# Performance work log

Measured on AMD Instinct MI355X. Metric: run time of the kernel, lower is better.

The kernel has to match this reference:

```python
import jax, jax.numpy as jnp
import numpy as np

EPS = 1e-5

def _conv3x3(x, w):
    # x: [n,c,h,w], w: [o,c,3,3], stride 1, padding 1 (SAME)
    return jax.lax.conv_general_dilated(x, w, (1, 1), 'SAME',
                                        dimension_numbers=('NCHW', 'OIHW', 'NCHW'))

def _bn(x, g, b, m, v):
    # inference-mode BatchNorm2d with running stats
    s = g / jnp.sqrt(v + EPS)
    return x * s[:, None, None] + (b - m * s)[:, None, None]

def _lrelu(x):
    return jnp.where(x > 0, x, 0.2 * x)

def _conv1x1(x, w, b):
    # w: [o,c] (1x1 conv kernel collapsed)
    return jnp.einsum('nchw,oc->nohw', x, w) + b[:, None, None]

def _conv_relu(x, w, g, b, m, v):
    return _lrelu(_bn(_conv3x3(x, w), g, b, m, v))

def _pam(f, Wq, bq, Wk, bk, Wv, bv, alpha):
    n, c, h, w = f.shape
    hw = h * w
    q = _conv1x1(f, Wq, bq).reshape(n, -1, hw)   # [n,cr,hw]
    k = _conv1x1(f, Wk, bk).reshape(n, -1, hw)   # [n,cr,hw]
    # attention[i,j] over spatial tokens, softmax along j
    attn = jax.nn.softmax(jnp.einsum('nci,ncj->nij', q, k), axis=-1)  # [n,hw,hw]
    v = _conv1x1(f, Wv, bv).reshape(n, c, hw)    # [n,c,hw]
    # torch: bmm(v, attn^T) -> out[:, :, i] = sum_j v[:, :, j] * attn[i, j]
    out = jnp.einsum('ncj,nij->nci', v, attn).reshape(n, c, h, w)
    return alpha * out + f

def _cam(f, W1, b1, W2, b2):
    s = jnp.mean(f, axis=(2, 3), keepdims=True)  # AdaptiveAvgPool2d(1)
    s = _lrelu(_conv1x1(s, W1, b1))
    s = jax.nn.sigmoid(_conv1x1(s, W2, b2))
    return f * s

def _upx2(x):
    n, c, h, w = x.shape
    return jax.image.resize(x, (n, c, 2 * h, 2 * w), 'bilinear')

def setup_inputs() -> dict:
    key = jax.random.key(0)
    ks = jax.random.split(key, 16)
    N, C, H, W_ = 4, 512, 64, 64
    CR, NC = C // 8, 64
    f32 = jnp.float32
    def nrm(k, shape, s=0.05):
        return jax.random.normal(k, shape, f32) * s
    return {
        'x': jax.random.normal(ks[0], (N, C, H, W_), f32),
        'W_pam_in': nrm(ks[1], (C, C, 3, 3)),
        'pam_gamma': jnp.ones((C,), f32), 'pam_beta': jnp.zeros((C,), f32),
        'pam_mean': nrm(ks[2], (C,)), 'pam_var': jax.random.uniform(ks[3], (C,), f32) + 0.5,
        'Wq': nrm(ks[4], (CR, C)), 'bq': jnp.zeros((CR,), f32),
        'Wk': nrm(ks[5], (CR, C)), 'bk': jnp.zeros((CR,), f32),
        'Wv': nrm(ks[6], (C, C)), 'bv': jnp.zeros((C,), f32),
        'alpha': nrm(ks[7], (1,), 1.0),
        'W_pam_out': nrm(ks[8], (NC, C)), 'b_pam_out': jnp.zeros((NC,), f32),
        'W_cam_in': nrm(ks[9], (C, C, 3, 3)),
        'cam_gamma': jnp.ones((C,), f32), 'cam_beta': jnp.zeros((C,), f32),
        'cam_mean': nrm(ks[10], (C,)), 'cam_var': jax.random.uniform(ks[11], (C,), f32) + 0.5,
        'Wc1': nrm(ks[12], (CR, C)), 'bc1': jnp.zeros((CR,), f32),
        'Wc2': nrm(ks[13], (C, CR)), 'bc2': jnp.zeros((C,), f32),
        'W_cam_out': nrm(ks[14], (NC, C)), 'b_cam_out': jnp.zeros((NC,), f32),
    }

def reference(x, W_pam_in, pam_gamma, pam_beta, pam_mean, pam_var,
              Wq, bq, Wk, bk, Wv, bv, alpha, W_pam_out, b_pam_out,
              W_cam_in, cam_gamma, cam_beta, cam_mean, cam_var,
              Wc1, bc1, Wc2, bc2, W_cam_out, b_cam_out):
    pam_feat = _conv_relu(x, W_pam_in, pam_gamma, pam_beta, pam_mean, pam_var)
    pam_feat = _pam(pam_feat, Wq, bq, Wk, bk, Wv, bv, alpha)
    pam_feat = _upx2(_conv1x1(pam_feat, W_pam_out, b_pam_out))
    cam_feat = _conv_relu(x, W_cam_in, cam_gamma, cam_beta, cam_mean, cam_var)
    cam_feat = _cam(cam_feat, Wc1, bc1, Wc2, bc2)
    cam_feat = _upx2(_conv1x1(cam_feat, W_cam_out, b_cam_out))
    return pam_feat + cam_feat
```

## Files before the change

### kernel.cpp

```cpp
#include <hip/hip_runtime.h>
#include <hip/hip_bf16.h>
#include <math.h>

#define N_  4
#define C_  512
#define H_  64
#define W_  64
#define HW_ 4096
#define CR_ 64
#define NC_ 64
#define EPSV 1e-5f

typedef __attribute__((ext_vector_type(8))) __bf16 bf16x8;
typedef __attribute__((ext_vector_type(4))) float f32x4;
typedef __hip_bfloat16 bf16s;

__device__ __forceinline__ unsigned short bfb(float f) {
    union { bf16s h; unsigned short u; } cv;
    cv.h = __float2bfloat16(f);
    return cv.u;
}

__device__ __forceinline__ int swz8(int row, int ch) {
    return row * 64 + ((ch ^ (row & 7)) << 3);
}

__global__ __launch_bounds__(256) void k_xpose(
    const float* __restrict__ x, bf16s* __restrict__ xbT)
{
    __shared__ float xs[64][65];
    const int tid = threadIdx.x;
    const int n = blockIdx.z, c0 = blockIdx.y * 64, p0 = blockIdx.x * 64;
    for (int e = tid; e < 4096; e += 256) {
        int ci = e >> 6, pi = e & 63;
        xs[ci][pi] = x[((size_t)(n*C_ + c0 + ci))*HW_ + p0 + pi];
    }
    __syncthreads();
    for (int e = tid; e < 4096; e += 256) {
        int pi = e >> 6, ci = e & 63;
        xbT[((size_t)n*HW_ + p0 + pi)*C_ + c0 + ci] = __float2bfloat16(xs[ci][pi]);
    }
}

__global__ __launch_bounds__(256) void k_wprep(
    const float* __restrict__ w, bf16s* __restrict__ wb)
{
    int e = blockIdx.x * 256 + threadIdx.x;
    int c = e & 511; int r = e >> 9;
    int tap = r % 9; int o = r / 9;
    wb[e] = __float2bfloat16(w[((size_t)o*C_ + c)*9 + tap]);
}

__global__ __launch_bounds__(256) void k_wcast(
    const float* __restrict__ in, bf16s* __restrict__ out, int nElem)
{
    int e = blockIdx.x * 256 + threadIdx.x;
    if (e < nElem) out[e] = __float2bfloat16(in[e]);
}

__global__ __launch_bounds__(256, 2) void k_conv3x3_mfma(
    const bf16s* __restrict__ xbT, const bf16s* __restrict__ wb,
    const float* __restrict__ gamma, const float* __restrict__ beta,
    const float* __restrict__ mean, const float* __restrict__ var,
    float* __restrict__ out, bf16s* __restrict__ featT,
    float* __restrict__ csum, int mode)
{
    __shared__ bf16s aL[3][128][40];
    __shared__ bf16s bL[132][40];
    const int tid = threadIdx.x;
    const int n  = blockIdx.z;
    const int o0 = blockIdx.y * 128;
    const int pt = blockIdx.x;
    const int y0 = pt * 2;
    const int lane = tid & 63;
    const int wid  = tid >> 6;
    const int wr = wid >> 1, wc = wid & 1;
    const int lr = lane & 15, cb = lane >> 4;

    const int ao  = tid >> 2;
    const int ac  = (tid & 3) * 8;
    const int t0  = tid >> 2;
    const int t1  = t0 + 64;
    const int t2  = t0 + 128;
    const int ry1 = t1 >= 66 ? 1 : 0;
    const int xi1 = t1 - (ry1 ? 66 : 0);

    f32x4 acc[4][4];
#pragma unroll
    for (int i = 0; i < 4; ++i)
#pragma unroll
        for (int j = 0; j < 4; ++j) acc[i][j] = (f32x4){0.f,0.f,0.f,0.f};

    int4 pA0, pA1, pA2, pA3, pA4, pA5, pB0, pB1, pB2;

#define CONV_AADDR(DXI, OHALF, C0, DYI) \
    (const int4*)(wb + ((size_t)(o0 + (OHALF) + ao)*9 + (DYI)*3 + (DXI))*C_ + (C0) + ac)

#define CONV_BLOAD(DST, RY, XI, C0, DYI, VALID)                               \
    {                                                                         \
        int row_ = y0 + (DYI) - 1 + (RY);                                     \
        int xc_  = (XI) - 1;                                                  \
        int4 v_ = {0,0,0,0};                                                  \
        if ((VALID) && row_ >= 0 && row_ < H_ && xc_ >= 0 && xc_ < W_)        \
            v_ = *(const int4*)(xbT +                                         \
                ((size_t)n*HW_ + row_*W_ + xc_)*C_ + (C0) + ac);              \
        DST = v_;                                                             \
    }

#define CONV_ISSUE(C0, DYI)                                                   \
    {                                                                         \
        pA0 = *CONV_AADDR(0,  0, C0, DYI);                                    \
        pA1 = *CONV_AADDR(0, 64, C0, DYI);                                    \
        pA2 = *CONV_AADDR(1,  0, C0, DYI);                                    \
        pA3 = *CONV_AADDR(1, 64, C0, DYI);                                    \
        pA4 = *CONV_AADDR(2,  0, C0, DYI);                                    \
        pA5 = *CONV_AADDR(2, 64, C0, DYI);                                    \
        CONV_BLOAD(pB0, 0, t0, C0, DYI, 1)                                    \
        CONV_BLOAD(pB1, ry1, xi1, C0, DYI, 1)                                 \
        CONV_BLOAD(pB2, 1, t2 - 66, C0, DYI, tid < 16)                        \
    }

    CONV_ISSUE(0, 0)
    int c0 = 0, dyi = 0;
    for (int it = 0; it < 48; ++it) {
        *(int4*)&aL[0][ao][ac]      = pA0;
        *(int4*)&aL[0][64 + ao][ac] = pA1;
        *(int4*)&aL[1][ao][ac]      = pA2;
        *(int4*)&aL[1][64 + ao][ac] = pA3;
        *(int4*)&aL[2][ao][ac]      = pA4;
        *(int4*)&aL[2][64 + ao][ac] = pA5;
        *(int4*)&bL[t0][ac] = pB0;
        *(int4*)&bL[t1][ac] = pB1;
        if (tid < 16) *(int4*)&bL[t2][ac] = pB2;
        __syncthreads();
        int nd = dyi + 1, nc = c0;
        if (nd == 3) { nd = 0; nc += 32; }
        if (it < 47) CONV_ISSUE(nc, nd)
#pragma unroll
        for (int dxi = 0; dxi < 3; ++dxi) {
            bf16x8 af[4], bfv[4];
#pragma unroll
            for (int fm = 0; fm < 4; ++fm)
                af[fm] = *(const bf16x8*)&aL[dxi][wr*64 + fm*16 + lr][cb*8];
#pragma unroll
            for (int fn = 0; fn < 4; ++fn) {
                int pg = wc*64 + fn*16 + lr;
                int ry = pg >> 6, xc = pg & 63;
                bfv[fn] = *(const bf16x8*)&bL[ry*66 + xc + dxi][cb*8];
            }
#pragma unroll
            for (int fm = 0; fm < 4; ++fm)
#pragma unroll
                for (int fn = 0; fn < 4; ++fn)
                    acc[fm][fn] = __builtin_amdgcn_mfma_f32_16x16x32_bf16(
                        af[fm], bfv[fn], acc[fm][fn], 0, 0, 0);
        }
        __syncthreads();
        c0 = nc; dyi = nd;
    }
#undef CONV_ISSUE
#undef CONV_BLOAD
#undef CONV_AADDR
#pragma unroll
    for (int fm = 0; fm < 4; ++fm) {
        float sc[4], sh[4];
        const int obase = o0 + wr*64 + fm*16 + cb*4;
#pragma unroll
        for (int r = 0; r < 4; ++r) {
            int o = obase + r;
            sc[r] = gamma[o] * rsqrtf(var[o] + EPSV);
            sh[r] = beta[o] - mean[o]*sc[r];
        }
        float ps[4] = {0.f, 0.f, 0.f, 0.f};
#pragma unroll
        for (int fn = 0; fn < 4; ++fn) {
            int pg = wc*64 + fn*16 + lr;
            int p  = pt*128 + pg;
            float vv[4];
#pragma unroll
            for (int r = 0; r < 4; ++r) {
                float t = fmaf(acc[fm][fn][r], sc[r], sh[r]);
                vv[r] = t > 0.f ? t : 0.2f*t;
                if (mode == 0)
                    out[((size_t)(n*C_ + obase + r))*HW_ + p] = vv[r];
                else
                    ps[r] += vv[r];
            }
            uint2 u;
            u.x = (unsigned)bfb(vv[0]) | ((unsigned)bfb(vv[1]) << 16);
            u.y = (unsigned)bfb(vv[2]) | ((unsigned)bfb(vv[3]) << 16);
            *(uint2*)&featT[((size_t)n*HW_ + p)*C_ + obase] = u;
        }
        if (mode != 0) {
#pragma unroll
            for (int r = 0; r < 4; ++r) {
                float s = ps[r];
                s += __shfl_xor(s, 1);
                s += __shfl_xor(s, 2);
                s += __shfl_xor(s, 4);
                s += __shfl_xor(s, 8);
                if (lr == 0) atomicAdd(&csum[n*C_ + obase + r], s);
            }
        }
    }
}

__global__ __launch_bounds__(256, 2) void k_gemm(
    const bf16s* __restrict__ A, const bf16s* __restrict__ Bt,
    const float* __restrict__ bias, const float* __restrict__ scale,
    void* __restrict__ outp, int O, int mode)
{
    __shared__ bf16s aL[64][40];
    __shared__ bf16s bL[256][40];
    const int tid = threadIdx.x;
    const int n  = blockIdx.z;
    const int p0 = blockIdx.x * 256;
    const int o0 = blockIdx.y * 64;
    const int lane = tid & 63;
    const int wid  = tid >> 6;
    const int lr = lane & 15, cb = lane >> 4;
    const int arow = tid >> 2, ach = (tid & 3) * 8;

    f32x4 acc[4][4];
#pragma unroll
    for (int i = 0; i < 4; ++i)
#pragma unroll
        for (int j = 0; j < 4; ++j) acc[i][j] = (f32x4){0.f,0.f,0.f,0.f};

    int4 pA, pB0, pB1, pB2, pB3;
    float4 pS0, pS1;

#define GEMM_ISSUE(C0)                                                        \
    {                                                                         \
        pA = *(const int4*)&A[(size_t)(o0 + arow)*C_ + (C0) + ach];           \
        if (scale) {                                                          \
            pS0 = *(const float4*)&scale[(size_t)n*C_ + (C0) + ach];          \
            pS1 = *(const float4*)&scale[(size_t)n*C_ + (C0) + ach + 4];      \
        }                                                                     \
        pB0 = *(const int4*)&Bt[((size_t)n*HW_ + p0 + arow      )*C_ + (C0) + ach]; \
        pB1 = *(const int4*)&Bt[((size_t)n*HW_ + p0 + arow +  64)*C_ + (C0) + ach]; \
        pB2 = *(const int4*)&Bt[((size_t)n*HW_ + p0 + arow + 128)*C_ + (C0) + ach]; \
        pB3 = *(const int4*)&Bt[((size_t)n*HW_ + p0 + arow + 192)*C_ + (C0) + ach]; \
    }

    GEMM_ISSUE(0)
    for (int c0 = 0; c0 < C_; c0 += 32) {
        if (scale) {
            const bf16s* sp = (const bf16s*)&pA;
            bf16s tmp[8];
            tmp[0] = __float2bfloat16(__bfloat162float(sp[0]) * pS0.x);
            tmp[1] = __float2bfloat16(__bfloat162float(sp[1]) * pS0.y);
            tmp[2] = __float2bfloat16(__bfloat162float(sp[2]) * pS0.z);
            tmp[3] = __float2bfloat16(__bfloat162float(sp[3]) * pS0.w);
            tmp[4] = __float2bfloat16(__bfloat162float(sp[4]) * pS1.x);
            tmp[5] = __float2bfloat16(__bfloat162float(sp[5]) * pS1.y);
            tmp[6] = __float2bfloat16(__bfloat162float(sp[6]) * pS1.z);
            tmp[7] = __float2bfloat16(__bfloat162float(sp[7]) * pS1.w);
            *(int4*)&aL[arow][ach] = *(int4*)tmp;
        } else {
            *(int4*)&aL[arow][ach] = pA;
        }
        *(int4*)&bL[arow      ][ach] = pB0;
        *(int4*)&bL[arow +  64][ach] = pB1;
        *(int4*)&bL[arow + 128][ach] = pB2;
        *(int4*)&bL[arow + 192][ach] = pB3;
        __syncthreads();
        if (c0 + 32 < C_) GEMM_ISSUE(c0 + 32)
        bf16x8 af[4], bfv[4];
#pragma unroll
        for (int fo = 0; fo < 4; ++fo)
            af[fo] = *(const bf16x8*)&aL[fo*16 + lr][cb*8];
#pragma unroll
        for (int fp = 0; fp < 4; ++fp)
            bfv[fp] = *(const bf16x8*)&bL[wid*64 + fp*16 + lr][cb*8];
#pragma unroll
        for (int fo = 0; fo < 4; ++fo)
#pragma unroll
            for (int fp = 0; fp < 4; ++fp)
                acc[fo][fp] = __builtin_amdgcn_mfma_f32_16x16x32_bf16(
                    af[fo], bfv[fp], acc[fo][fp], 0, 0, 0);
        __syncthreads();
    }
#undef GEMM_ISSUE
#pragma unroll
    for (int fo = 0; fo < 4; ++fo) {
        const int obase = o0 + fo*16 + cb*4;
        float bv[4];
#pragma unroll
        for (int r = 0; r < 4; ++r) bv[r] = bias[obase + r];
#pragma unroll
        for (int fp = 0; fp < 4; ++fp) {
            int p = p0 + wid*64 + fp*16 + lr;
            float v[4];
#pragma unroll
            for (int r = 0; r < 4; ++r) v[r] = acc[fo][fp][r] + bv[r];
            if (mode == 1) {
                uint2 u;
                u.x = (unsigned)bfb(v[0]) | ((unsigned)bfb(v[1]) << 16);
                u.y = (unsigned)bfb(v[2]) | ((unsigned)bfb(v[3]) << 16);
                *(uint2*)&((bf16s*)outp)[((size_t)n*HW_ + p)*O + (obase - o0)] = u;
            } else if (mode == 2) {
#pragma unroll
                for (int r = 0; r < 4; ++r)
                    ((bf16s*)outp)[((size_t)(n*O + obase + r))*HW_ + p] =
                        __float2bfloat16(v[r]);
            } else {
#pragma unroll
                for (int r = 0; r < 4; ++r)
                    ((float*)outp)[((size_t)(n*O + obase + r))*HW_ + p] = v[r];
            }
        }
    }
}

__global__ __launch_bounds__(256) void k_rowstats_mfma(
    const bf16s* __restrict__ qb, const bf16s* __restrict__ kb,
    float* __restrict__ rowm, float* __restrict__ rowl)
{
    __shared__ bf16s qs[4096];
    __shared__ bf16s ks[4096];
    const int tid = threadIdx.x;
    const int lid = blockIdx.x + (blockIdx.y << 6) + (blockIdx.z << 8);
    const int n  = lid & 3;
    const int jz = (lid >> 2) & 1;
    const int i0 = (lid >> 3) << 6;
    const int lane = tid & 63;
    const int wid  = tid >> 6;
    const int lr = lane & 15, cb = lane >> 4;

    for (int e = tid; e < 512; e += 256) {
        int row = e >> 3, ch = e & 7;
        *(int4*)&qs[swz8(row, ch)] =
            *(const int4*)&qb[((size_t)n*HW_ + i0 + row)*CR_ + ch*8];
    }
    const int krow = tid >> 3, kch = tid & 7;
    const bf16s* kbase = kb + (size_t)n*HW_*CR_ + (size_t)jz*2048*CR_ + kch*8;
    int4 kreg0 = *(const int4*)(kbase + (size_t)krow*CR_);
    int4 kreg1 = *(const int4*)(kbase + (size_t)(krow + 32)*CR_);
    __syncthreads();
    bf16x8 bq[2];
#pragma unroll
    for (int kk = 0; kk < 2; ++kk)
        bq[kk] = *(const bf16x8*)&qs[swz8(wid*16 + lr, kk*4 + cb)];

    float m_t = -INFINITY, l_t = 0.f;
    for (int t = 0; t < 32; ++t) {
        __syncthreads();
        *(int4*)&ks[swz8(krow, kch)] = kreg0;
        *(int4*)&ks[swz8(krow + 32, kch)] = kreg1;
        if (t < 31) {
            kreg0 = *(const int4*)(kbase + (size_t)((t+1)*64 + krow)*CR_);
            kreg1 = *(const int4*)(kbase + (size_t)((t+1)*64 + krow + 32)*CR_);
        }
        __syncthreads();
        f32x4 sv[4];
#pragma unroll
        for (int fj = 0; fj < 4; ++fj) {
            f32x4 s = (f32x4){0.f,0.f,0.f,0.f};
#pragma unroll
            for (int kk = 0; kk < 2; ++kk) {
                bf16x8 ak = *(const bf16x8*)&ks[swz8(fj*16 + lr, kk*4 + cb)];
                s = __builtin_amdgcn_mfma_f32_16x16x32_bf16(ak, bq[kk], s, 0, 0, 0);
            }
            sv[fj] = s;
        }
        float mx = m_t;
#pragma unroll
        for (int fj = 0; fj < 4; ++fj)
#pragma unroll
            for (int r = 0; r < 4; ++r) mx = fmaxf(mx, sv[fj][r]);
        float sum = 0.f;
#pragma unroll
        for (int fj = 0; fj < 4; ++fj)
#pragma unroll
            for (int r = 0; r < 4; ++r) sum += __expf(sv[fj][r] - mx);
        l_t = l_t * __expf(m_t - mx) + sum;
        m_t = mx;
    }
#pragma unroll
    for (int mask = 16; mask <= 32; mask <<= 1) {
        float mo = __shfl_xor(m_t, mask);
        float lo = __shfl_xor(l_t, mask);
        float m2 = fmaxf(m_t, mo);
        l_t = l_t * __expf(m_t - m2) + lo * __expf(mo - m2);
        m_t = m2;
    }
    if (cb == 0) {
        rowm[((size_t)jz*N_ + n)*HW_ + i0 + wid*16 + lr] = m_t;
        rowl[((size_t)jz*N_ + n)*HW_ + i0 + wid*16 + lr] = l_t;
    }
}

__global__ __launch_bounds__(256, 4) void k_pv_mfma(
    const bf16s* __restrict__ qb, const bf16s* __restrict__ kb,
    const bf16s* __restrict__ vb, const float* __restrict__ rowm,
    const float* __restrict__ rowl, const float* __restrict__ alpha,
    const float* __restrict__ feat, bf16s* __restrict__ featT)
{
    __shared__ bf16s ks[4096];
    __shared__ bf16s qps[4096];
    const int tid = threadIdx.x;
    const int lid = blockIdx.x + (blockIdx.y << 6) + (blockIdx.z << 8);
    const int k8  = lid & 7;
    const int n   = k8 >> 1;
    const int cc0 = (((lid >> 3) & 1) * 2 + (k8 & 1)) << 7;
    const int i0  = (lid >> 4) << 6;
    const int lane = tid & 63;
    const int wid  = tid >> 6;
    const int lr = lane & 15, cb = lane >> 4;

    for (int e = tid; e < 512; e += 256) {
        int row = e >> 3, ch = e & 7;
        *(int4*)&qps[swz8(row, ch)] =
            *(const int4*)&qb[((size_t)n*HW_ + i0 + row)*CR_ + ch*8];
    }
    const int krow = tid >> 3, kch = tid & 7;
    const bf16s* kbase = kb + (size_t)n*HW_*CR_ + kch*8;
    int4 kreg0 = *(const int4*)(kbase + (size_t)krow*CR_);
    int4 kreg1 = *(const int4*)(kbase + (size_t)(krow + 32)*CR_);
    __syncthreads();
    bf16x8 bq[2];
#pragma unroll
    for (int kk = 0; kk < 2; ++kk)
        bq[kk] = *(const bf16x8*)&qps[swz8(wid*16 + lr, kk*4 + cb)];

    const size_t sidx = (size_t)n*HW_ + i0 + wid*16 + lr;
    const float m0 = rowm[sidx], m1 = rowm[sidx + (size_t)N_*HW_];
    const float l0 = rowl[sidx], l1 = rowl[sidx + (size_t)N_*HW_];
    const float mreg = fmaxf(m0, m1);
    const float rinv = 1.f / (l0*__expf(m0 - mreg) + l1*__expf(m1 - mreg));
    const float al = alpha[0];

    f32x4 acc[2][4];
#pragma unroll
    for (int i = 0; i < 2; ++i)
#pragma unroll
        for (int j = 0; j < 4; ++j) acc[i][j] = (f32x4){0.f,0.f,0.f,0.f};

    const bf16s* vbase = vb + ((size_t)(n*C_ + cc0 + wid*32))*HW_;

    for (int jt = 0; jt < 64; ++jt) {
        *(int4*)&ks[swz8(krow, kch)] = kreg0;
        *(int4*)&ks[swz8(krow + 32, kch)] = kreg1;
        if (jt < 63) {
            kreg0 = *(const int4*)(kbase + (size_t)((jt+1)*64 + krow)*CR_);
            kreg1 = *(const int4*)(kbase + (size_t)((jt+1)*64 + krow + 32)*CR_);
        }
        __syncthreads();
#pragma unroll
        for (int fj = 0; fj < 4; ++fj) {
            f32x4 s = (f32x4){0.f,0.f,0.f,0.f};
#pragma unroll
            for (int kk = 0; kk < 2; ++kk) {
                bf16x8 ak = *(const bf16x8*)&ks[swz8(fj*16 + lr, kk*4 + cb)];
                s = __builtin_amdgcn_mfma_f32_16x16x32_bf16(ak, bq[kk], s, 0, 0, 0);
            }
            unsigned short b[4];
#pragma unroll
            for (int r = 0; r < 4; ++r)
                b[r] = bfb(__expf(s[r] - mreg) * rinv);
            uint2 u;
            u.x = (unsigned)b[0] | ((unsigned)b[1] << 16);
            u.y = (unsigned)b[2] | ((unsigned)b[3] << 16);
            *(uint2*)&qps[swz8(wid*16 + lr, fj*2 + (cb >> 1)) + (cb & 1)*4] = u;
        }
        __syncthreads();
        const bf16s* vj = vbase + jt*64;
#pragma unroll
        for (int kk2 = 0; kk2 < 2; ++kk2) {
            bf16x8 vf[2], pa[4];
#pragma unroll
            for (int fc2 = 0; fc2 < 2; ++fc2)
                vf[fc2] = *(const bf16x8*)(vj + (size_t)(fc2*16 + lr)*HW_
                                              + kk2*32 + cb*8);
#pragma unroll
            for (int fi = 0; fi < 4; ++fi)
                pa[fi] = *(const bf16x8*)&qps[swz8(fi*16 + lr, kk2*4 + cb)];
#pragma unroll
            for (int fc2 = 0; fc2 < 2; ++fc2)
#pragma unroll
                for (int fi = 0; fi < 4; ++fi)
                    acc[fc2][fi] = __builtin_amdgcn_mfma_f32_16x16x32_bf16(
                        vf[fc2], pa[fi], acc[fc2][fi], 0, 0, 0);
        }
    }
#pragma unroll
    for (int fc2 = 0; fc2 < 2; ++fc2) {
        const int ccl = wid*32 + fc2*16 + cb*4;
#pragma unroll
        for (int fi = 0; fi < 4; ++fi) {
            const int p = i0 + fi*16 + lr;
            const float* fp = &feat[((size_t)(n*C_ + cc0 + ccl))*HW_ + p];
            float v0 = fmaf(al, acc[fc2][fi][0], fp[0]);
            float v1 = fmaf(al, acc[fc2][fi][1], fp[(size_t)HW_]);
            float v2 = fmaf(al, acc[fc2][fi][2], fp[(size_t)2*HW_]);
            float v3 = fmaf(al, acc[fc2][fi][3], fp[(size_t)3*HW_]);
            uint2 u;
            u.x = (unsigned)bfb(v0) | ((unsigned)bfb(v1) << 16);
            u.y = (unsigned)bfb(v2) | ((unsigned)bfb(v3) << 16);
            *(uint2*)&featT[((size_t)n*HW_ + p)*C_ + cc0 + ccl] = u;
        }
    }
}

__global__ __launch_bounds__(64) void k_cmlp(
    const float* __restrict__ s0, const float* __restrict__ Wc1,
    const float* __restrict__ bc1, const float* __restrict__ Wc2,
    const float* __restrict__ bc2, float* __restrict__ s2)
{
    const int n = blockIdx.x, tid = threadIdx.x;
    __shared__ float s1s[64];
    float a = 0.f;
    for (int c = 0; c < C_; ++c)
        a = fmaf(Wc1[(size_t)tid*C_ + c], s0[n*C_ + c] * (1.f/HW_), a);
    a += bc1[tid];
    a = a > 0.f ? a : 0.2f*a;
    s1s[tid] = a;
    __syncthreads();
    for (int c = tid; c < C_; c += 64) {
        float b = 0.f;
        for (int i = 0; i < CR_; ++i) b = fmaf(Wc2[(size_t)c*CR_ + i], s1s[i], b);
        b += bc2[c];
        s2[n*C_ + c] = 1.f / (1.f + __expf(-b));
    }
}

__global__ __launch_bounds__(256) void k_up(
    const float* __restrict__ pl, const float* __restrict__ cl,
    float* __restrict__ out)
{
    int idx = blockIdx.x * 256 + threadIdx.x;
    int ox = idx & 127; int rest = idx >> 7;
    int oy = rest & 127; rest >>= 7;
    int o  = rest & 63;  int n = rest >> 6;
    float fy = oy*0.5f - 0.25f;
    float fx = ox*0.5f - 0.25f;
    int y0 = (int)floorf(fy); float wy = fy - y0;
    int x0 = (int)floorf(fx); float wx = fx - x0;
    int y0c = y0 < 0 ? 0 : y0;      int y1c = y0+1 > 63 ? 63 : y0+1;
    int x0c = x0 < 0 ? 0 : x0;      int x1c = x0+1 > 63 ? 63 : x0+1;
    const float* a = pl + ((size_t)(n*NC_ + o))*HW_;
    const float* b = cl + ((size_t)(n*NC_ + o))*HW_;
    float v00 = a[y0c*64+x0c] + b[y0c*64+x0c];
    float v01 = a[y0c*64+x1c] + b[y0c*64+x1c];
    float v10 = a[y1c*64+x0c] + b[y1c*64+x0c];
    float v11 = a[y1c*64+x1c] + b[y1c*64+x1c];
    out[idx] = (1.f-wy)*((1.f-wx)*v00 + wx*v01) + wy*((1.f-wx)*v10 + wx*v11);
}

extern "C" void kernel_launch(void* const* d_in, const int* in_sizes, int n_in,
                              void* d_out, int out_size, void* d_ws, size_t ws_size,
                              hipStream_t stream)
{
    const float* x         = (const float*)d_in[0];
    const float* W_pam_in  = (const float*)d_in[1];
    const float* pam_g     = (const float*)d_in[2];
    const float* pam_b     = (const float*)d_in[3];
    const float* pam_m     = (const float*)d_in[4];
    const float* pam_v     = (const float*)d_in[5];
    const float* Wq        = (const float*)d_in[6];
    const float* bq        = (const float*)d_in[7];
    const float* Wk        = (const float*)d_in[8];
    const float* bk        = (const float*)d_in[9];
    const float* Wv        = (const float*)d_in[10];
    const float* bv        = (const float*)d_in[11];
    const float* alpha     = (const float*)d_in[12];
    const float* W_pam_out = (const float*)d_in[13];
    const float* b_pam_out = (const float*)d_in[14];
    const float* W_cam_in  = (const float*)d_in[15];
    const float* cam_g     = (const float*)d_in[16];
    const float* cam_b     = (const float*)d_in[17];
    const float* cam_m     = (const float*)d_in[18];
    const float* cam_v     = (const float*)d_in[19];
    const float* Wc1       = (const float*)d_in[20];
    const float* bc1       = (const float*)d_in[21];
    const float* Wc2       = (const float*)d_in[22];
    const float* bc2       = (const float*)d_in[23];
    const float* W_cam_out = (const float*)d_in[24];
    const float* b_cam_out = (const float*)d_in[25];

    float* feat    = (float*)d_ws;
    float* pam_low = feat    + 8388608;
    float* rowm    = pam_low + 1048576;
    float* rowl    = rowm    + 32768;
    float* s0      = rowl    + 32768;
    float* s2      = s0      + 2048;
    bf16s* xbT     = (bf16s*)(s2 + 2048);
    bf16s* featTb  = xbT + 8388608;
    bf16s* vb      = featTb + 8388608;
    bf16s* qb      = vb + 8388608;
    bf16s* kb      = qb + 1048576;
    bf16s* wbp     = kb + 1048576;
    bf16s* Wqb     = wbp + 2359296;
    bf16s* Wkb     = Wqb + 32768;
    bf16s* Wvb     = Wkb + 32768;
    bf16s* Wpob    = Wvb + 262144;
    bf16s* Wcob    = Wpob + 32768;
    float* cam_low = (float*)qb;

    dim3 b256(256);
    k_xpose<<<dim3(64,8,4), b256, 0, stream>>>(x, xbT);
    k_wcast<<<dim3(128), b256, 0, stream>>>(Wq, Wqb, 32768);
    k_wcast<<<dim3(128), b256, 0, stream>>>(Wk, Wkb, 32768);
    k_wcast<<<dim3(1024), b256, 0, stream>>>(Wv, Wvb, 262144);
    k_wcast<<<dim3(128), b256, 0, stream>>>(W_pam_out, Wpob, 32768);
    k_wcast<<<dim3(128), b256, 0, stream>>>(W_cam_out, Wcob, 32768);
    hipMemsetAsync(s0, 0, 2048*sizeof(float), stream);
    k_wprep<<<dim3(9216), b256, 0, stream>>>(W_pam_in, wbp);
    k_conv3x3_mfma<<<dim3(32,4,4), b256, 0, stream>>>(
        xbT, wbp, pam_g, pam_b, pam_m, pam_v, feat, featTb, nullptr, 0);
    k_gemm<<<dim3(16,1,4), b256, 0, stream>>>(Wqb, featTb, bq, nullptr, qb, 64, 1);
    k_gemm<<<dim3(16,1,4), b256, 0, stream>>>(Wkb, featTb, bk, nullptr, kb, 64, 1);
    k_gemm<<<dim3(16,8,4), b256, 0, stream>>>(Wvb, featTb, bv, nullptr, vb, 512, 2);
    k_rowstats_mfma<<<dim3(64,4,2), b256, 0, stream>>>(qb, kb, rowm, rowl);
    k_pv_mfma<<<dim3(64,4,4), b256, 0, stream>>>(
        qb, kb, vb, rowm, rowl, alpha, feat, featTb);
    k_gemm<<<dim3(16,1,4), b256, 0, stream>>>(
        Wpob, featTb, b_pam_out, nullptr, pam_low, 64, 0);
    k_wprep<<<dim3(9216), b256, 0, stream>>>(W_cam_in, wbp);
    k_conv3x3_mfma<<<dim3(32,4,4), b256, 0, stream>>>(
        xbT, wbp, cam_g, cam_b, cam_m, cam_v, feat, featTb, s0, 1);
    k_cmlp<<<dim3(4), dim3(64), 0, stream>>>(s0, Wc1, bc1, Wc2, bc2, s2);
    k_gemm<<<dim3(16,1,4), b256, 0, stream>>>(
        Wcob, featTb, b_cam_out, s2, cam_low, 64, 0);
    k_up<<<dim3(16384), b256, 0, stream>>>(pam_low, cam_low, (float*)d_out);
}
```

Measured before the change: 482.7 us.

## Double-buffer K and P tiles and software-pipeline attention loops

Both attention kernels now keep two LDS buffers for the K tile, so each iteration has one barrier instead of two. The PV kernel also double-buffers the probability tile: the P·V MFMAs for the previous tile are interleaved with the QK scores and exp for the current tile, and V fragments are prefetched one iteration ahead in registers. The aim is to hide global-load and barrier latency and overlap the exp work with matrix ops. In exchange, LDS use and register pressure go up, which could lower occupancy under the launch_bounds(256,4) setting.

After: 482.2 us. No clear change (-0.1%).

```diff
diff --git a/kernel.cpp b/kernel.cpp
--- a/kernel.cpp
+++ b/kernel.cpp
@@ -318,7 +318,7 @@
     float* __restrict__ rowm, float* __restrict__ rowl)
 {
     __shared__ bf16s qs[4096];
-    __shared__ bf16s ks[4096];
+    __shared__ bf16s ks[2][4096];
     const int tid = threadIdx.x;
     const int lid = blockIdx.x + (blockIdx.y << 6) + (blockIdx.z << 8);
     const int n  = lid & 3;
@@ -337,6 +337,10 @@
     const bf16s* kbase = kb + (size_t)n*HW_*CR_ + (size_t)jz*2048*CR_ + kch*8;
     int4 kreg0 = *(const int4*)(kbase + (size_t)krow*CR_);
     int4 kreg1 = *(const int4*)(kbase + (size_t)(krow + 32)*CR_);
+    *(int4*)&ks[0][swz8(krow, kch)] = kreg0;
+    *(int4*)&ks[0][swz8(krow + 32, kch)] = kreg1;
+    kreg0 = *(const int4*)(kbase + (size_t)(64 + krow)*CR_);
+    kreg1 = *(const int4*)(kbase + (size_t)(64 + krow + 32)*CR_);
     __syncthreads();
     bf16x8 bq[2];
 #pragma unroll
@@ -345,24 +349,25 @@
 
     float m_t = -INFINITY, l_t = 0.f;
     for (int t = 0; t < 32; ++t) {
-        __syncthreads();
-        *(int4*)&ks[swz8(krow, kch)] = kreg0;
-        *(int4*)&ks[swz8(krow + 32, kch)] = kreg1;
-        if (t < 31) {
-            kreg0 = *(const int4*)(kbase + (size_t)((t+1)*64 + krow)*CR_);
-            kreg1 = *(const int4*)(kbase + (size_t)((t+1)*64 + krow + 32)*CR_);
-        }
-        __syncthreads();
+        const bf16s* kst = ks[t & 1];
         f32x4 sv[4];
 #pragma unroll
         for (int fj = 0; fj < 4; ++fj) {
             f32x4 s = (f32x4){0.f,0.f,0.f,0.f};
 #pragma unroll
             for (int kk = 0; kk < 2; ++kk) {
-                bf16x8 ak = *(const bf16x8*)&ks[swz8(fj*16 + lr, kk*4 + cb)];
+                bf16x8 ak = *(const bf16x8*)&kst[swz8(fj*16 + lr, kk*4 + cb)];
                 s = __builtin_amdgcn_mfma_f32_16x16x32_bf16(ak, bq[kk], s, 0, 0, 0);
             }
             sv[fj] = s;
+        }
+        if (t < 31) {
+            *(int4*)&ks[(t + 1) & 1][swz8(krow, kch)] = kreg0;
+            *(int4*)&ks[(t + 1) & 1][swz8(krow + 32, kch)] = kreg1;
+            if (t < 30) {
+                kreg0 = *(const int4*)(kbase + (size_t)((t+2)*64 + krow)*CR_);
+                kreg1 = *(const int4*)(kbase + (size_t)((t+2)*64 + krow + 32)*CR_);
+            }
         }
         float mx = m_t;
 #pragma unroll
@@ -376,6 +381,7 @@
             for (int r = 0; r < 4; ++r) sum += __expf(sv[fj][r] - mx);
         l_t = l_t * __expf(m_t - mx) + sum;
         m_t = mx;
+        __syncthreads();
     }
 #pragma unroll
     for (int mask = 16; mask <= 32; mask <<= 1) {
@@ -397,8 +403,8 @@
     const float* __restrict__ rowl, const float* __restrict__ alpha,
     const float* __restrict__ feat, bf16s* __restrict__ featT)
 {
-    __shared__ bf16s ks[4096];
-    __shared__ bf16s qps[4096];
+    __shared__ bf16s ks[2][4096];
+    __shared__ bf16s ps[2][4096];
     const int tid = threadIdx.x;
     const int lid = blockIdx.x + (blockIdx.y << 6) + (blockIdx.z << 8);
     const int k8  = lid & 7;
@@ -411,7 +417,7 @@
 
     for (int e = tid; e < 512; e += 256) {
         int row = e >> 3, ch = e & 7;
-        *(int4*)&qps[swz8(row, ch)] =
+        *(int4*)&ks[0][swz8(row, ch)] =
             *(const int4*)&qb[((size_t)n*HW_ + i0 + row)*CR_ + ch*8];
     }
     const int krow = tid >> 3, kch = tid & 7;
@@ -422,7 +428,7 @@
     bf16x8 bq[2];
 #pragma unroll
     for (int kk = 0; kk < 2; ++kk)
-        bq[kk] = *(const bf16x8*)&qps[swz8(wid*16 + lr, kk*4 + cb)];
+        bq[kk] = *(const bf16x8*)&ks[0][swz8(wid*16 + lr, kk*4 + cb)];
 
     const size_t sidx = (size_t)n*HW_ + i0 + wid*16 + lr;
     const float m0 = rowm[sidx], m1 = rowm[sidx + (size_t)N_*HW_];
@@ -430,6 +436,12 @@
     const float mreg = fmaxf(m0, m1);
     const float rinv = 1.f / (l0*__expf(m0 - mreg) + l1*__expf(m1 - mreg));
     const float al = alpha[0];
+    __syncthreads();
+    *(int4*)&ks[0][swz8(krow, kch)] = kreg0;
+    *(int4*)&ks[0][swz8(krow + 32, kch)] = kreg1;
+    kreg0 = *(const int4*)(kbase + (size_t)(64 + krow)*CR_);
+    kreg1 = *(const int4*)(kbase + (size_t)(64 + krow + 32)*CR_);
+    __syncthreads();
 
     f32x4 acc[2][4];
 #pragma unroll
@@ -438,50 +450,92 @@
         for (int j = 0; j < 4; ++j) acc[i][j] = (f32x4){0.f,0.f,0.f,0.f};
 
     const bf16s* vbase = vb + ((size_t)(n*C_ + cc0 + wid*32))*HW_;
+    bf16x8 vc0, vc1, vc2, vc3, vn0, vn1, vn2, vn3;
 
     for (int jt = 0; jt < 64; ++jt) {
-        *(int4*)&ks[swz8(krow, kch)] = kreg0;
-        *(int4*)&ks[swz8(krow + 32, kch)] = kreg1;
+        const bf16s* vj = vbase + jt*64;
+        vn0 = *(const bf16x8*)(vj + (size_t)(     lr)*HW_      + cb*8);
+        vn1 = *(const bf16x8*)(vj + (size_t)(16 + lr)*HW_      + cb*8);
+        vn2 = *(const bf16x8*)(vj + (size_t)(     lr)*HW_ + 32 + cb*8);
+        vn3 = *(const bf16x8*)(vj + (size_t)(16 + lr)*HW_ + 32 + cb*8);
+        if (jt > 0) {
+            const bf16s* pp = ps[(jt - 1) & 1];
+            bf16x8 pa[4];
+#pragma unroll
+            for (int fi = 0; fi < 4; ++fi)
+                pa[fi] = *(const bf16x8*)&pp[swz8(fi*16 + lr, cb)];
+#pragma unroll
+            for (int fi = 0; fi < 4; ++fi) {
+                acc[0][fi] = __builtin_amdgcn_mfma_f32_16x16x32_bf16(
+                    vc0, pa[fi], acc[0][fi], 0, 0, 0);
+                acc[1][fi] = __builtin_amdgcn_mfma_f32_16x16x32_bf16(
+                    vc1, pa[fi], acc[1][fi], 0, 0, 0);
+            }
+#pragma unroll
+            for (int fi = 0; fi < 4; ++fi)
+                pa[fi] = *(const bf16x8*)&pp[swz8(fi*16 + lr, 4 + cb)];
+#pragma unroll
+            for (int fi = 0; fi < 4; ++fi) {
+                acc[0][fi] = __builtin_amdgcn_mfma_f32_16x16x32_bf16(
+                    vc2, pa[fi], acc[0][fi], 0, 0, 0);
+                acc[1][fi] = __builtin_amdgcn_mfma_f32_16x16x32_bf16(
+                    vc3, pa[fi], acc[1][fi], 0, 0, 0);
+            }
+        }
+        {
+            const bf16s* kst = ks[jt & 1];
+            bf16s* pst = ps[jt & 1];
+#pragma unroll
+            for (int fj = 0; fj < 4; ++fj) {
+                f32x4 s = (f32x4){0.f,0.f,0.f,0.f};
+#pragma unroll
+                for (int kk = 0; kk < 2; ++kk) {
+                    bf16x8 ak = *(const bf16x8*)&kst[swz8(fj*16 + lr, kk*4 + cb)];
+                    s = __builtin_amdgcn_mfma_f32_16x16x32_bf16(ak, bq[kk], s, 0, 0, 0);
+                }
+                unsigned short b[4];
+#pragma unroll
+                for (int r = 0; r < 4; ++r)
+                    b[r] = bfb(__expf(s[r] - mreg) * rinv);
+                uint2 u;
+                u.x = (unsigned)b[0] | ((unsigned)b[1] << 16);
+                u.y = (unsigned)b[2] | ((unsigned)b[3] << 16);
+                *(uint2*)&pst[swz8(wid*16 + lr, fj*2 + (cb >> 1)) + (cb & 1)*4] = u;
+            }
+        }
         if (jt < 63) {
-            kreg0 = *(const int4*)(kbase + (size_t)((jt+1)*64 + krow)*CR_);
-            kreg1 = *(const int4*)(kbase + (size_t)((jt+1)*64 + krow + 32)*CR_);
-        }
+            *(int4*)&ks[(jt + 1) & 1][swz8(krow, kch)] = kreg0;
+            *(int4*)&ks[(jt + 1) & 1][swz8(krow + 32, kch)] = kreg1;
+            if (jt < 62) {
+                kreg0 = *(const int4*)(kbase + (size_t)((jt+2)*64 + krow)*CR_);
+                kreg1 = *(const int4*)(kbase + (size_t)((jt+2)*64 + krow + 32)*CR_);
+            }
+        }
+        vc0 = vn0; vc1 = vn1; vc2 = vn2; vc3 = vn3;
         __syncthreads();
-#pragma unroll
-        for (int fj = 0; fj < 4; ++fj) {
-            f32x4 s = (f32x4){0.f,0.f,0.f,0.f};
-#pragma unroll
-            for (int kk = 0; kk < 2; ++kk) {
-                bf16x8 ak = *(const bf16x8*)&ks[swz8(fj*16 + lr, kk*4 + cb)];
-                s = __builtin_amdgcn_mfma_f32_16x16x32_bf16(ak, bq[kk], s, 0, 0, 0);
-            }
-            unsigned short b[4];
-#pragma unroll
-            for (int r = 0; r < 4; ++r)
-                b[r] = bfb(__expf(s[r] - mreg) * rinv);
-            uint2 u;
-            u.x = (unsigned)b[0] | ((unsigned)b[1] << 16);
-            u.y = (unsigned)b[2] | ((unsigned)b[3] << 16);
-            *(uint2*)&qps[swz8(wid*16 + lr, fj*2 + (cb >> 1)) + (cb & 1)*4] = u;
-        }
-        __syncthreads();
-        const bf16s* vj = vbase + jt*64;
-#pragma unroll
-        for (int kk2 = 0; kk2 < 2; ++kk2) {
-            bf16x8 vf[2], pa[4];
-#pragma unroll
-            for (int fc2 = 0; fc2 < 2; ++fc2)
-                vf[fc2] = *(const bf16x8*)(vj + (size_t)(fc2*16 + lr)*HW_
-                                              + kk2*32 + cb*8);
-#pragma unroll
-            for (int fi = 0; fi < 4; ++fi)
-                pa[fi] = *(const bf16x8*)&qps[swz8(fi*16 + lr, kk2*4 + cb)];
-#pragma unroll
-            for (int fc2 = 0; fc2 < 2; ++fc2)
-#pragma unroll
-                for (int fi = 0; fi < 4; ++fi)
-                    acc[fc2][fi] = __builtin_amdgcn_mfma_f32_16x16x32_bf16(
-                        vf[fc2], pa[fi], acc[fc2][fi], 0, 0, 0);
+    }
+    {
+        const bf16s* pp = ps[63 & 1];
+        bf16x8 pa[4];
+#pragma unroll
+        for (int fi = 0; fi < 4; ++fi)
+            pa[fi] = *(const bf16x8*)&pp[swz8(fi*16 + lr, cb)];
+#pragma unroll
+        for (int fi = 0; fi < 4; ++fi) {
+            acc[0][fi] = __builtin_amdgcn_mfma_f32_16x16x32_bf16(
+                vc0, pa[fi], acc[0][fi], 0, 0, 0);
+            acc[1][fi] = __builtin_amdgcn_mfma_f32_16x16x32_bf16(
+                vc1, pa[fi], acc[1][fi], 0, 0, 0);
+        }
+#pragma unroll
+        for (int fi = 0; fi < 4; ++fi)
+            pa[fi] = *(const bf16x8*)&pp[swz8(fi*16 + lr, 4 + cb)];
+#pragma unroll
+        for (int fi = 0; fi < 4; ++fi) {
+            acc[0][fi] = __builtin_amdgcn_mfma_f32_16x16x32_bf16(
+                vc2, pa[fi], acc[0][fi], 0, 0, 0);
+            acc[1][fi] = __builtin_amdgcn_mfma_f32_16x16x32_bf16(
+                vc3, pa[fi], acc[1][fi], 0, 0, 0);
         }
     }
 #pragma unroll
```

## Load K fragments directly to registers and software-pipeline PV with double-buffered P

Applied to the files above, without the earlier changes.

Both attention kernels now read K fragments from global memory straight into MFMA operand registers instead of staging them through shared memory, which removes the K LDS tile and its barriers. The row-stats kernel splits the key range four ways instead of two, giving twice as many blocks, and the PV kernel merges four partial max/sum pairs. The PV kernel double-buffers the probability tile in LDS so the P·V MFMAs for the previous tile overlap with the QK and exp work for the current tile, with one barrier per iteration and s_setprio around the MFMA bursts. In exchange it uses more registers and does redundant uncoalesced global K reads per wave, relying on cache hits.

After: 722.3 us. +49.6%, slower.

```diff
diff --git a/kernel.cpp b/kernel.cpp
--- a/kernel.cpp
+++ b/kernel.cpp
@@ -318,12 +318,11 @@
     float* __restrict__ rowm, float* __restrict__ rowl)
 {
     __shared__ bf16s qs[4096];
-    __shared__ bf16s ks[4096];
     const int tid = threadIdx.x;
     const int lid = blockIdx.x + (blockIdx.y << 6) + (blockIdx.z << 8);
     const int n  = lid & 3;
-    const int jz = (lid >> 2) & 1;
-    const int i0 = (lid >> 3) << 6;
+    const int jz = (lid >> 2) & 3;
+    const int i0 = (lid >> 4) << 6;
     const int lane = tid & 63;
     const int wid  = tid >> 6;
     const int lr = lane & 15, cb = lane >> 4;
@@ -333,47 +332,58 @@
         *(int4*)&qs[swz8(row, ch)] =
             *(const int4*)&qb[((size_t)n*HW_ + i0 + row)*CR_ + ch*8];
     }
-    const int krow = tid >> 3, kch = tid & 7;
-    const bf16s* kbase = kb + (size_t)n*HW_*CR_ + (size_t)jz*2048*CR_ + kch*8;
-    int4 kreg0 = *(const int4*)(kbase + (size_t)krow*CR_);
-    int4 kreg1 = *(const int4*)(kbase + (size_t)(krow + 32)*CR_);
+    const bf16s* kp = kb + ((size_t)n*HW_ + jz*1024 + lr)*CR_ + cb*8;
+    bf16x8 kc0, kc1, kc2, kc3, kc4, kc5, kc6, kc7;
+    kc0 = *(const bf16x8*)(kp);
+    kc1 = *(const bf16x8*)(kp + 32);
+    kc2 = *(const bf16x8*)(kp + 16*CR_);
+    kc3 = *(const bf16x8*)(kp + 16*CR_ + 32);
+    kc4 = *(const bf16x8*)(kp + 32*CR_);
+    kc5 = *(const bf16x8*)(kp + 32*CR_ + 32);
+    kc6 = *(const bf16x8*)(kp + 48*CR_);
+    kc7 = *(const bf16x8*)(kp + 48*CR_ + 32);
     __syncthreads();
-    bf16x8 bq[2];
-#pragma unroll
-    for (int kk = 0; kk < 2; ++kk)
-        bq[kk] = *(const bf16x8*)&qs[swz8(wid*16 + lr, kk*4 + cb)];
+    bf16x8 bq0 = *(const bf16x8*)&qs[swz8(wid*16 + lr, cb)];
+    bf16x8 bq1 = *(const bf16x8*)&qs[swz8(wid*16 + lr, 4 + cb)];
 
     float m_t = -INFINITY, l_t = 0.f;
-    for (int t = 0; t < 32; ++t) {
-        __syncthreads();
-        *(int4*)&ks[swz8(krow, kch)] = kreg0;
-        *(int4*)&ks[swz8(krow + 32, kch)] = kreg1;
-        if (t < 31) {
-            kreg0 = *(const int4*)(kbase + (size_t)((t+1)*64 + krow)*CR_);
-            kreg1 = *(const int4*)(kbase + (size_t)((t+1)*64 + krow + 32)*CR_);
-        }
-        __syncthreads();
-        f32x4 sv[4];
-#pragma unroll
-        for (int fj = 0; fj < 4; ++fj) {
-            f32x4 s = (f32x4){0.f,0.f,0.f,0.f};
-#pragma unroll
-            for (int kk = 0; kk < 2; ++kk) {
-                bf16x8 ak = *(const bf16x8*)&ks[swz8(fj*16 + lr, kk*4 + cb)];
-                s = __builtin_amdgcn_mfma_f32_16x16x32_bf16(ak, bq[kk], s, 0, 0, 0);
-            }
-            sv[fj] = s;
+    for (int t = 0; t < 16; ++t) {
+        f32x4 sv0, sv1, sv2, sv3;
+        sv0 = (f32x4){0.f,0.f,0.f,0.f};
+        sv0 = __builtin_amdgcn_mfma_f32_16x16x32_bf16(kc0, bq0, sv0, 0, 0, 0);
+        sv0 = __builtin_amdgcn_mfma_f32_16x16x32_bf16(kc1, bq1, sv0, 0, 0, 0);
+        sv1 = (f32x4){0.f,0.f,0.f,0.f};
+        sv1 = __builtin_amdgcn_mfma_f32_16x16x32_bf16(kc2, bq0, sv1, 0, 0, 0);
+        sv1 = __builtin_amdgcn_mfma_f32_16x16x32_bf16(kc3, bq1, sv1, 0, 0, 0);
+        sv2 = (f32x4){0.f,0.f,0.f,0.f};
+        sv2 = __builtin_amdgcn_mfma_f32_16x16x32_bf16(kc4, bq0, sv2, 0, 0, 0);
+        sv2 = __builtin_amdgcn_mfma_f32_16x16x32_bf16(kc5, bq1, sv2, 0, 0, 0);
+        sv3 = (f32x4){0.f,0.f,0.f,0.f};
+        sv3 = __builtin_amdgcn_mfma_f32_16x16x32_bf16(kc6, bq0, sv3, 0, 0, 0);
+        sv3 = __builtin_amdgcn_mfma_f32_16x16x32_bf16(kc7, bq1, sv3, 0, 0, 0);
+        if (t < 15) {
+            const bf16s* kn = kp + (size_t)(t + 1)*64*CR_;
+            kc0 = *(const bf16x8*)(kn);
+            kc1 = *(const bf16x8*)(kn + 32);
+            kc2 = *(const bf16x8*)(kn + 16*CR_);
+            kc3 = *(const bf16x8*)(kn + 16*CR_ + 32);
+            kc4 = *(const bf16x8*)(kn + 32*CR_);
+            kc5 = *(const bf16x8*)(kn + 32*CR_ + 32);
+            kc6 = *(const bf16x8*)(kn + 48*CR_);
+            kc7 = *(const bf16x8*)(kn + 48*CR_ + 32);
         }
         float mx = m_t;
 #pragma unroll
-        for (int fj = 0; fj < 4; ++fj)
-#pragma unroll
-            for (int r = 0; r < 4; ++r) mx = fmaxf(mx, sv[fj][r]);
+        for (int r = 0; r < 4; ++r) {
+            mx = fmaxf(mx, sv0[r]); mx = fmaxf(mx, sv1[r]);
+            mx = fmaxf(mx, sv2[r]); mx = fmaxf(mx, sv3[r]);
+        }
         float sum = 0.f;
 #pragma unroll
-        for (int fj = 0; fj < 4; ++fj)
-#pragma unroll
-            for (int r = 0; r < 4; ++r) sum += __expf(sv[fj][r] - mx);
+        for (int r = 0; r < 4; ++r) {
+            sum += __expf(sv0[r] - mx); sum += __expf(sv1[r] - mx);
+            sum += __expf(sv2[r] - mx); sum += __expf(sv3[r] - mx);
+        }
         l_t = l_t * __expf(m_t - mx) + sum;
         m_t = mx;
     }
@@ -397,8 +407,7 @@
     const float* __restrict__ rowl, const float* __restrict__ alpha,
     const float* __restrict__ feat, bf16s* __restrict__ featT)
 {
-    __shared__ bf16s ks[4096];
-    __shared__ bf16s qps[4096];
+    __shared__ bf16s ps[2][4096];
     const int tid = threadIdx.x;
     const int lid = blockIdx.x + (blockIdx.y << 6) + (blockIdx.z << 8);
     const int k8  = lid & 7;
@@ -411,25 +420,34 @@
 
     for (int e = tid; e < 512; e += 256) {
         int row = e >> 3, ch = e & 7;
-        *(int4*)&qps[swz8(row, ch)] =
+        *(int4*)&ps[0][swz8(row, ch)] =
             *(const int4*)&qb[((size_t)n*HW_ + i0 + row)*CR_ + ch*8];
     }
-    const int krow = tid >> 3, kch = tid & 7;
-    const bf16s* kbase = kb + (size_t)n*HW_*CR_ + kch*8;
-    int4 kreg0 = *(const int4*)(kbase + (size_t)krow*CR_);
-    int4 kreg1 = *(const int4*)(kbase + (size_t)(krow + 32)*CR_);
+    const bf16s* kp = kb + ((size_t)n*HW_ + lr)*CR_ + cb*8;
+    bf16x8 kc0, kc1, kc2, kc3, kc4, kc5, kc6, kc7;
+    kc0 = *(const bf16x8*)(kp);
+    kc1 = *(const bf16x8*)(kp + 32);
+    kc2 = *(const bf16x8*)(kp + 16*CR_);
+    kc3 = *(const bf16x8*)(kp + 16*CR_ + 32);
+    kc4 = *(const bf16x8*)(kp + 32*CR_);
+    kc5 = *(const bf16x8*)(kp + 32*CR_ + 32);
+    kc6 = *(const bf16x8*)(kp + 48*CR_);
+    kc7 = *(const bf16x8*)(kp + 48*CR_ + 32);
     __syncthreads();
-    bf16x8 bq[2];
-#pragma unroll
-    for (int kk = 0; kk < 2; ++kk)
-        bq[kk] = *(const bf16x8*)&qps[swz8(wid*16 + lr, kk*4 + cb)];
+    bf16x8 bq0 = *(const bf16x8*)&ps[0][swz8(wid*16 + lr, cb)];
+    bf16x8 bq1 = *(const bf16x8*)&ps[0][swz8(wid*16 + lr, 4 + cb)];
 
     const size_t sidx = (size_t)n*HW_ + i0 + wid*16 + lr;
-    const float m0 = rowm[sidx], m1 = rowm[sidx + (size_t)N_*HW_];
-    const float l0 = rowl[sidx], l1 = rowl[sidx + (size_t)N_*HW_];
-    const float mreg = fmaxf(m0, m1);
-    const float rinv = 1.f / (l0*__expf(m0 - mreg) + l1*__expf(m1 - mreg));
+    const float m0 = rowm[sidx], m1 = rowm[sidx + 16384];
+    const float m2 = rowm[sidx + 32768], m3 = rowm[sidx + 49152];
+    const float mreg = fmaxf(fmaxf(m0, m1), fmaxf(m2, m3));
+    const float lsum = rowl[sidx]          * __expf(m0 - mreg)
+                     + rowl[sidx + 16384]  * __expf(m1 - mreg)
+                     + rowl[sidx + 32768]  * __expf(m2 - mreg)
+                     + rowl[sidx + 49152]  * __expf(m3 - mreg);
+    const float rinv = 1.f / lsum;
     const float al = alpha[0];
+    __syncthreads();
 
     f32x4 acc[2][4];
 #pragma unroll
@@ -438,51 +456,109 @@
         for (int j = 0; j < 4; ++j) acc[i][j] = (f32x4){0.f,0.f,0.f,0.f};
 
     const bf16s* vbase = vb + ((size_t)(n*C_ + cc0 + wid*32))*HW_;
+    bf16x8 vc0, vc1, vc2, vc3;
 
     for (int jt = 0; jt < 64; ++jt) {
-        *(int4*)&ks[swz8(krow, kch)] = kreg0;
-        *(int4*)&ks[swz8(krow + 32, kch)] = kreg1;
+        if (jt > 0) {
+            const bf16s* pp = ps[(jt - 1) & 1];
+            bf16x8 pa0 = *(const bf16x8*)&pp[swz8(     lr, cb)];
+            bf16x8 pa1 = *(const bf16x8*)&pp[swz8(16 + lr, cb)];
+            bf16x8 pa2 = *(const bf16x8*)&pp[swz8(32 + lr, cb)];
+            bf16x8 pa3 = *(const bf16x8*)&pp[swz8(48 + lr, cb)];
+            __builtin_amdgcn_s_setprio(1);
+            acc[0][0] = __builtin_amdgcn_mfma_f32_16x16x32_bf16(vc0, pa0, acc[0][0], 0, 0, 0);
+            acc[1][0] = __builtin_amdgcn_mfma_f32_16x16x32_bf16(vc1, pa0, acc[1][0], 0, 0, 0);
+            acc[0][1] = __builtin_amdgcn_mfma_f32_16x16x32_bf16(vc0, pa1, acc[0][1], 0, 0, 0);
+            acc[1][1] = __builtin_amdgcn_mfma_f32_16x16x32_bf16(vc1, pa1, acc[1][1], 0, 0, 0);
+            acc[0][2] = __builtin_amdgcn_mfma_f32_16x16x32_bf16(vc0, pa2, acc[0][2], 0, 0, 0);
+            acc[1][2] = __builtin_amdgcn_mfma_f32_16x16x32_bf16(vc1, pa2, acc[1][2], 0, 0, 0);
+            acc[0][3] = __builtin_amdgcn_mfma_f32_16x16x32_bf16(vc0, pa3, acc[0][3], 0, 0, 0);
+            acc[1][3] = __builtin_amdgcn_mfma_f32_16x16x32_bf16(vc1, pa3, acc[1][3], 0, 0, 0);
+            __builtin_amdgcn_s_setprio(0);
+            pa0 = *(const bf16x8*)&pp[swz8(     lr, 4 + cb)];
+            pa1 = *(const bf16x8*)&pp[swz8(16 + lr, 4 + cb)];
+            pa2 = *(const bf16x8*)&pp[swz8(32 + lr, 4 + cb)];
+            pa3 = *(const bf16x8*)&pp[swz8(48 + lr, 4 + cb)];
+            __builtin_amdgcn_s_setprio(1);
+            acc[0][0] = __builtin_amdgcn_mfma_f32_16x16x32_bf16(vc2, pa0, acc[0][0], 0, 0, 0);
+            acc[1][0] = __builtin_amdgcn_mfma_f32_16x16x32_bf16(vc3, pa0, acc[1][0], 0, 0, 0);
+            acc[0][1] = __builtin_amdgcn_mfma_f32_16x16x32_bf16(vc2, pa1, acc[0][1], 0, 0, 0);
+            acc[1][1] = __builtin_amdgcn_mfma_f32_16x16x32_bf16(vc3, pa1, acc[1][1], 0, 0, 0);
+            acc[0][2] = __builtin_amdgcn_mfma_f32_16x16x32_bf16(vc2, pa2, acc[0][2], 0, 0, 0);
+            acc[1][2] = __builtin_amdgcn_mfma_f32_16x16x32_bf16(vc3, pa2, acc[1][2], 0, 0, 0);
+            acc[0][3] = __builtin_amdgcn_mfma_f32_16x16x32_bf16(vc2, pa3, acc[0][3], 0, 0, 0);
+            acc[1][3] = __builtin_amdgcn_mfma_f32_16x16x32_bf16(vc3, pa3, acc[1][3], 0, 0, 0);
+            __builtin_amdgcn_s_setprio(0);
+        }
+        {
+            const bf16s* vj = vbase + jt*64;
+            vc0 = *(const bf16x8*)(vj + (size_t)(     lr)*HW_      + cb*8);
+            vc1 = *(const bf16x8*)(vj + (size_t)(16 + lr)*HW_      + cb*8);
+            vc2 = *(const bf16x8*)(vj + (size_t)(     lr)*HW_ + 32 + cb*8);
+            vc3 = *(const bf16x8*)(vj + (size_t)(16 + lr)*HW_ + 32 + cb*8);
+        }
+        {
+            bf16s* pst = ps[jt & 1];
+            f32x4 s;
+#define PV_STEXP(FJ, KA, KB)                                                  \
+            s = (f32x4){0.f,0.f,0.f,0.f};                                     \
+            s = __builtin_amdgcn_mfma_f32_16x16x32_bf16(KA, bq0, s, 0, 0, 0); \
+            s = __builtin_amdgcn_mfma_f32_16x16x32_bf16(KB, bq1, s, 0, 0, 0); \
+            {                                                                 \
+                unsigned short b0 = bfb(__expf(s[0] - mreg) * rinv);          \
+                unsigned short b1 = bfb(__expf(s[1] - mreg) * rinv);          \
+                unsigned short b2 = bfb(__expf(s[2] - mreg) * rinv);          \
+                unsigned short b3 = bfb(__expf(s[3] - mreg) * rinv);          \
+                uint2 u;                                                      \
+                u.x = (unsigned)b0 | ((unsigned)b1 << 16);                    \
+                u.y = (unsigned)b2 | ((unsigned)b3 << 16);                    \
+                *(uint2*)&pst[swz8(wid*16 + lr, FJ*2 + (cb >> 1)) + (cb & 1)*4] = u; \
+            }
+            PV_STEXP(0, kc0, kc1)
+            PV_STEXP(1, kc2, kc3)
+            PV_STEXP(2, kc4, kc5)
+            PV_STEXP(3, kc6, kc7)
+#undef PV_STEXP
+        }
         if (jt < 63) {
-            kreg0 = *(const int4*)(kbase + (size_t)((jt+1)*64 + krow)*CR_);
-            kreg1 = *(const int4*)(kbase + (size_t)((jt+1)*64 + krow + 32)*CR_);
+            const bf16s* kn = kp + (size_t)(jt + 1)*64*CR_;
+            kc0 = *(const bf16x8*)(kn);
+            kc1 = *(const bf16x8*)(kn + 32);
+            kc2 = *(const bf16x8*)(kn + 16*CR_);
+            kc3 = *(const bf16x8*)(kn + 16*CR_ + 32);
+            kc4 = *(const bf16x8*)(kn + 32*CR_);
+            kc5 = *(const bf16x8*)(kn + 32*CR_ + 32);
+            kc6 = *(const bf16x8*)(kn + 48*CR_);
+            kc7 = *(const bf16x8*)(kn + 48*CR_ + 32);
         }
         __syncthreads();
-#pragma unroll
-        for (int fj = 0; fj < 4; ++fj) {
-            f32x4 s = (f32x4){0.f,0.f,0.f,0.f};
-#pragma unroll
-            for (int kk = 0; kk < 2; ++kk) {
-                bf16x8 ak = *(const bf16x8*)&ks[swz8(fj*16 + lr, kk*4 + cb)];
-                s = __builtin_amdgcn_mfma_f32_16x16x32_bf16(ak, bq[kk], s, 0, 0, 0);
-            }
-            unsigned short b[4];
-#pragma unroll
-            for (int r = 0; r < 4; ++r)
-                b[r] = bfb(__expf(s[r] - mreg) * rinv);
-            uint2 u;
-            u.x = (unsigned)b[0] | ((unsigned)b[1] << 16);
-            u.y = (unsigned)b[2] | ((unsigned)b[3] << 16);
-            *(uint2*)&qps[swz8(wid*16 + lr, fj*2 + (cb >> 1)) + (cb & 1)*4] = u;
-        }
-        __syncthreads();
-        const bf16s* vj = vbase + jt*64;
-#pragma unroll
-        for (int kk2 = 0; kk2 < 2; ++kk2) {
-            bf16x8 vf[2], pa[4];
-#pragma unroll
-            for (int fc2 = 0; fc2 < 2; ++fc2)
-                vf[fc2] = *(const bf16x8*)(vj + (size_t)(fc2*16 + lr)*HW_
-                                              + kk2*32 + cb*8);
-#pragma unroll
-            for (int fi = 0; fi < 4; ++fi)
-                pa[fi] = *(const bf16x8*)&qps[swz8(fi*16 + lr, kk2*4 + cb)];
-#pragma unroll
-            for (int fc2 = 0; fc2 < 2; ++fc2)
-#pragma unroll
-                for (int fi = 0; fi < 4; ++fi)
-                    acc[fc2][fi] = __builtin_amdgcn_mfma_f32_16x16x32_bf16(
-                        vf[fc2], pa[fi], acc[fc2][fi], 0, 0, 0);
-        }
+    }
+    {
+        const bf16s* pp = ps[1];
+        bf16x8 pa0 = *(const bf16x8*)&pp[swz8(     lr, cb)];
+        bf16x8 pa1 = *(const bf16x8*)&pp[swz8(16 + lr, cb)];
+        bf16x8 pa2 = *(const bf16x8*)&pp[swz8(32 + lr, cb)];
+        bf16x8 pa3 = *(const bf16x8*)&pp[swz8(48 + lr, cb)];
+        acc[0][0] = __builtin_amdgcn_mfma_f32_16x16x32_bf16(vc0, pa0, acc[0][0], 0, 0, 0);
+        acc[1][0] = __builtin_amdgcn_mfma_f32_16x16x32_bf16(vc1, pa0, acc[1][0], 0, 0, 0);
+        acc[0][1] = __builtin_amdgcn_mfma_f32_16x16x32_bf16(vc0, pa1, acc[0][1], 0, 0, 0);
+        acc[1][1] = __builtin_amdgcn_mfma_f32_16x16x32_bf16(vc1, pa1, acc[1][1], 0, 0, 0);
+        acc[0][2] = __builtin_amdgcn_mfma_f32_16x16x32_bf16(vc0, pa2, acc[0][2], 0, 0, 0);
+        acc[1][2] = __builtin_amdgcn_mfma_f32_16x16x32_bf16(vc1, pa2, acc[1][2], 0, 0, 0);
+        acc[0][3] = __builtin_amdgcn_mfma_f32_16x16x32_bf16(vc0, pa3, acc[0][3], 0, 0, 0);
+        acc[1][3] = __builtin_amdgcn_mfma_f32_16x16x32_bf16(vc1, pa3, acc[1][3], 0, 0, 0);
+        pa0 = *(const bf16x8*)&pp[swz8(     lr, 4 + cb)];
+        pa1 = *(const bf16x8*)&pp[swz8(16 + lr, 4 + cb)];
+        pa2 = *(const bf16x8*)&pp[swz8(32 + lr, 4 + cb)];
+        pa3 = *(const bf16x8*)&pp[swz8(48 + lr, 4 + cb)];
+        acc[0][0] = __builtin_amdgcn_mfma_f32_16x16x32_bf16(vc2, pa0, acc[0][0], 0, 0, 0);
+        acc[1][0] = __builtin_amdgcn_mfma_f32_16x16x32_bf16(vc3, pa0, acc[1][0], 0, 0, 0);
+        acc[0][1] = __builtin_amdgcn_mfma_f32_16x16x32_bf16(vc2, pa1, acc[0][1], 0, 0, 0);
+        acc[1][1] = __builtin_amdgcn_mfma_f32_16x16x32_bf16(vc3, pa1, acc[1][1], 0, 0, 0);
+        acc[0][2] = __builtin_amdgcn_mfma_f32_16x16x32_bf16(vc2, pa2, acc[0][2], 0, 0, 0);
+        acc[1][2] = __builtin_amdgcn_mfma_f32_16x16x32_bf16(vc3, pa2, acc[1][2], 0, 0, 0);
+        acc[0][3] = __builtin_amdgcn_mfma_f32_16x16x32_bf16(vc2, pa3, acc[0][3], 0, 0, 0);
+        acc[1][3] = __builtin_amdgcn_mfma_f32_16x16x32_bf16(vc3, pa3, acc[1][3], 0, 0, 0);
     }
 #pragma unroll
     for (int fc2 = 0; fc2 < 2; ++fc2) {
@@ -582,8 +658,8 @@
     float* feat    = (float*)d_ws;
     float* pam_low = feat    + 8388608;
     float* rowm    = pam_low + 1048576;
-    float* rowl    = rowm    + 32768;
-    float* s0      = rowl    + 32768;
+    float* rowl    = rowm    + 65536;
+    float* s0      = rowl    + 65536;
     float* s2      = s0      + 2048;
     bf16s* xbT     = (bf16s*)(s2 + 2048);
     bf16s* featTb  = xbT + 8388608;
@@ -612,7 +688,7 @@
     k_gemm<<<dim3(16,1,4), b256, 0, stream>>>(Wqb, featTb, bq, nullptr, qb, 64, 1);
     k_gemm<<<dim3(16,1,4), b256, 0, stream>>>(Wkb, featTb, bk, nullptr, kb, 64, 1);
     k_gemm<<<dim3(16,8,4), b256, 0, stream>>>(Wvb, featTb, bv, nullptr, vb, 512, 2);
-    k_rowstats_mfma<<<dim3(64,4,2), b256, 0, stream>>>(qb, kb, rowm, rowl);
+    k_rowstats_mfma<<<dim3(64,4,4), b256, 0, stream>>>(qb, kb, rowm, rowl);
     k_pv_mfma<<<dim3(64,4,4), b256, 0, stream>>>(
         qb, kb, vb, rowm, rowl, alpha, feat, featTb);
     k_gemm<<<dim3(16,1,4), b256, 0, stream>>>(
```
